# Kernel tuning notes

Hardware: AMD Instinct MI355X
Metric: run time of the kernel (lower is better)

## Reference

```python
import jax, jax.numpy as jnp
import numpy as np

DIM = 768
N_HEAD = 12
HEAD_DIM = 64
INNER = N_HEAD * HEAD_DIM
SCALE = HEAD_DIM ** -0.5


def setup_inputs() -> dict:
    key = jax.random.key(0)
    ks = jax.random.split(key, 12)
    B, Sf, St = 4, 2048, 2048
    from_tensor = jax.random.normal(ks[0], (B, Sf, DIM), dtype=jnp.float32)
    to_tensor = jax.random.normal(ks[1], (B, St, DIM), dtype=jnp.float32)
    attention_mask = jax.random.randint(ks[2], (B, Sf, St), 0, 2, dtype=jnp.int32)
    # Dense layers: kernel ~ RandomNormal (stddev 0.05, keras default), bias zeros
    def kern(k, fan_in, fan_out):
        return 0.05 * jax.random.normal(k, (fan_in, fan_out), dtype=jnp.float32)
    return {
        "from_tensor": from_tensor,
        "to_tensor": to_tensor,
        "attention_mask": attention_mask,
        "Wq": kern(ks[3], DIM, INNER), "bq": jnp.zeros((INNER,), jnp.float32),
        "Wk": kern(ks[4], DIM, INNER), "bk": jnp.zeros((INNER,), jnp.float32),
        "Wv": kern(ks[5], DIM, INNER), "bv": jnp.zeros((INNER,), jnp.float32),
        "Wo": kern(ks[6], INNER, DIM), "bo": jnp.zeros((DIM,), jnp.float32),
    }


def reference(from_tensor, to_tensor, attention_mask, Wq, bq, Wk, bk, Wv, bv, Wo, bo):
    B, Sf, _ = from_tensor.shape
    St = to_tensor.shape[1]
    # projections -> [B, S, n_head, head_dim] -> [B, n_head, S, head_dim]
    def split_heads(x, S):
        return x.reshape(B, S, N_HEAD, HEAD_DIM).transpose(0, 2, 1, 3)
    q = split_heads(from_tensor @ Wq + bq, Sf) * SCALE
    k = split_heads(to_tensor @ Wk + bk, St)
    v = split_heads(to_tensor @ Wv + bv, St)
    # scores [B, H, Sf, St]
    scores = jnp.einsum('bhik,bhjk->bhij', q, k)
    adder = (1.0 - attention_mask.astype(jnp.float32)) * -10000.0
    scores = scores + adder[:, None, :, :]
    probs = jax.nn.softmax(scores, axis=-1)
    out = jnp.einsum('bhij,bhjk->bhik', probs, v)  # [B, H, Sf, Dh]
    out = out.transpose(0, 2, 1, 3).reshape(B, Sf, INNER)
    return out @ Wo + bo
```

## Files before the change

kernel.cpp:

```cpp
#include <hip/hip_runtime.h>
#include <stdint.h>

#define DIM 768
#define NH 12
#define HD 64
#define BSZ 4
#define SEQ 2048
#define MROWS (BSZ*SEQ)

typedef __attribute__((ext_vector_type(8))) short v8s;
typedef __attribute__((ext_vector_type(4))) float v4f;
typedef __attribute__((ext_vector_type(8))) _Float16 v8h;
typedef __attribute__((ext_vector_type(2))) __fp16 v2fp;

__device__ __forceinline__ uint16_t f2bf(float x) {
  union { float f; uint32_t u; } v; v.f = x;
  uint32_t r = v.u + 0x7fffu + ((v.u >> 16) & 1u);
  return (uint16_t)(r >> 16);
}

#if __has_builtin(__builtin_amdgcn_cvt_pk_bf16_f32)
typedef __attribute__((ext_vector_type(2))) __bf16 v2bf;
__device__ __forceinline__ uint32_t pack_bf16(float a, float b) {
  union { v2bf v; uint32_t u; } c;
  c.v = __builtin_amdgcn_cvt_pk_bf16_f32(a, b);
  return c.u;
}
#else
__device__ __forceinline__ uint32_t pack_bf16(float a, float b) {
  return (uint32_t)f2bf(a) | ((uint32_t)f2bf(b) << 16);
}
#endif

__device__ __forceinline__ uint32_t pack_f16(float a, float b) {
#if __has_builtin(__builtin_amdgcn_cvt_pkrtz)
  union { v2fp h; uint32_t u; } c;
  c.h = __builtin_amdgcn_cvt_pkrtz(a, b);
  return c.u;
#else
  union { _Float16 h[2]; uint32_t u; } c;
  c.h[0] = (_Float16)a; c.h[1] = (_Float16)b; return c.u;
#endif
}

__device__ __forceinline__ float fexp2(float x) {
#if __has_builtin(__builtin_amdgcn_exp2f)
  return __builtin_amdgcn_exp2f(x);
#else
  return exp2f(x);
#endif
}

__device__ __forceinline__ void gl16(const void* g, void* l) {
  __builtin_amdgcn_global_load_lds(
      (const __attribute__((address_space(1))) unsigned int*)g,
      (__attribute__((address_space(3))) unsigned int*)l, 16, 0, 0);
}

__device__ __forceinline__ void pipe_sync() {
  asm volatile("s_waitcnt vmcnt(0)" ::: "memory");
  __builtin_amdgcn_s_barrier();
  __builtin_amdgcn_sched_barrier(0);
}

#define CVT_BLKS  12288
#define WT_BLKS   2304
__global__ __launch_bounds__(256) void prepass_kernel(
    const float* __restrict__ from_t, const float* __restrict__ to_t,
    uint16_t* __restrict__ Xf, uint16_t* __restrict__ Xt,
    const float* __restrict__ Wq, const float* __restrict__ Wk,
    const float* __restrict__ Wv, const float* __restrict__ Wo,
    uint16_t* __restrict__ WT)
{
  __shared__ float tile[32][33];
  int blk = blockIdx.x, tid = threadIdx.x;
  if (blk < CVT_BLKS) {
    int n4 = MROWS * DIM / 4;
    int i = blk * 256 + tid;
    const float* src = (i < n4) ? from_t : to_t;
    uint16_t* dst = (i < n4) ? Xf : Xt;
    int j = (i < n4) ? i : i - n4;
    float4 v = ((const float4*)src)[j];
    uint2 o;
    o.x = pack_bf16(v.x, v.y);
    o.y = pack_bf16(v.z, v.w);
    ((uint2*)dst)[j] = o;
  } else {
    int r = blk - CVT_BLKS;
    int z = r / 576, rem = r - z * 576;
    int by = rem / 24, bx = rem - by * 24;
    const float* src = (z==0) ? Wq : (z==1) ? Wk : (z==2) ? Wv : Wo;
    uint16_t* dst = WT + (size_t)z * DIM * DIM;
    int tx = tid & 31, ty = tid >> 5;
    int x  = bx * 32 + tx;
    int y0 = by * 32;
    for (int jj = ty; jj < 32; jj += 8)
      tile[jj][tx] = src[(size_t)(y0 + jj) * DIM + x];
    __syncthreads();
    int xo = y0 + tx;
    for (int jj = ty; jj < 32; jj += 8)
      dst[(size_t)(bx * 32 + jj) * DIM + xo] = f2bf(tile[tx][jj]);
  }
}

__global__ __launch_bounds__(256) void gemm_kernel(
    const uint16_t* __restrict__ Xf, const uint16_t* __restrict__ Xt,
    const uint16_t* __restrict__ WT, const uint16_t* __restrict__ AO,
    const float* __restrict__ bq, const float* __restrict__ bk,
    const float* __restrict__ bv, const float* __restrict__ bo,
    uint16_t* __restrict__ Qw, uint16_t* __restrict__ Kw, uint16_t* __restrict__ Vw,
    float* __restrict__ Out, const int* __restrict__ maski,
    unsigned long long* __restrict__ Mbits, int mode_base)
{
  __shared__ alignas(16) uint16_t As[2][128 * 32];
  __shared__ alignas(16) uint16_t Bs[2][128 * 32];
  int tid = threadIdx.x;

  if (mode_base == 0 && blockIdx.z == 3) {
    int wave = tid >> 6, lane = tid & 63;
    int wid = (blockIdx.y * 64 + blockIdx.x) * 4 + wave;
    const int NWAVES = 1536, NW = BSZ * 32 * SEQ;
    for (int w0 = wid; w0 < NW; w0 += 4 * NWAVES) {
      int m[4]; int wv[4];
      #pragma unroll
      for (int u = 0; u < 4; u++) {
        int w = w0 + u * NWAVES;
        wv[u] = w;
        m[u] = 0;
        if (w < NW) {
          int b  = w >> 16;
          int q  = (w >> 5) & 2047;
          int kt = w & 31;
          m[u] = maski[((size_t)b * SEQ + q) * SEQ + kt * 64 + lane];
        }
      }
      #pragma unroll
      for (int u = 0; u < 4; u++) {
        int w = wv[u];
        if (w < NW) {
          unsigned long long bits = __ballot(m[u] != 0);
          if (lane == 0) {
            int b  = w >> 16;
            int q  = (w >> 5) & 2047;
            int kt = w & 31;
            Mbits[((size_t)b * 32 + kt) * SEQ + q] = bits;
          }
        }
      }
    }
    return;
  }

  int mode = mode_base + blockIdx.z;
  const uint16_t* A = (mode == 0) ? Xf : (mode == 3 ? AO : Xt);
  const uint16_t* W = WT + (size_t)mode * DIM * DIM;
  const float* bias = (mode == 0) ? bq : (mode == 1) ? bk : (mode == 2) ? bv : bo;

  int m0 = blockIdx.x * 128, n0 = blockIdx.y * 128;
  int wave = tid >> 6, lane = tid & 63, lr = lane & 15, quad = lane >> 4;
  int wm = (wave >> 1) * 64, wn = (wave & 1) * 64;

  int seg = (lane & 3) ^ ((lane >> 3) & 3);
  const uint16_t* agl = A + (size_t)(m0 + wave * 32 + (lane >> 2)) * DIM + seg * 8;
  const uint16_t* bgl = W + (size_t)(n0 + wave * 32 + (lane >> 2)) * DIM + seg * 8;
  int lb = wave * 1024;
  int ck = (lr >> 1) & 3;

  v4f acc[4][4];
  v4f vz = {0.f, 0.f, 0.f, 0.f};
  #pragma unroll
  for (int i = 0; i < 4; i++)
    #pragma unroll
    for (int j = 0; j < 4; j++) acc[i][j] = vz;

  gl16(agl,            &As[0][lb]);
  gl16(agl + 16 * DIM, &As[0][lb + 512]);
  gl16(bgl,            &Bs[0][lb]);
  gl16(bgl + 16 * DIM, &Bs[0][lb + 512]);
  pipe_sync();

  int cur = 0;
  const int NT = DIM / 32;
  for (int t = 0; t < NT; ++t) {
    if (t + 1 < NT) {
      int kn = (t + 1) * 32;
      gl16(agl + kn,            &As[cur ^ 1][lb]);
      gl16(agl + kn + 16 * DIM, &As[cur ^ 1][lb + 512]);
      gl16(bgl + kn,            &Bs[cur ^ 1][lb]);
      gl16(bgl + kn + 16 * DIM, &Bs[cur ^ 1][lb + 512]);
    }
    v8s af[4], bfr[4];
    #pragma unroll
    for (int i = 0; i < 4; i++)
      af[i] = *(const v8s*)&As[cur][(wm + i * 16 + lr) * 32 + ((quad ^ ck) << 3)];
    #pragma unroll
    for (int j = 0; j < 4; j++)
      bfr[j] = *(const v8s*)&Bs[cur][(wn + j * 16 + lr) * 32 + ((quad ^ ck) << 3)];
    #pragma unroll
    for (int i = 0; i < 4; i++)
      #pragma unroll
      for (int j = 0; j < 4; j++)
        acc[i][j] = __builtin_amdgcn_mfma_f32_16x16x32_bf16(af[i], bfr[j], acc[i][j], 0, 0, 0);
    if (t + 1 < NT) pipe_sync();
    cur ^= 1;
  }

  float bj[4];
  #pragma unroll
  for (int j = 0; j < 4; j++) bj[j] = bias[n0 + wn + j * 16 + lr];

  if (mode == 3) {
    #pragma unroll
    for (int i = 0; i < 4; i++) {
      int m = m0 + wm + i * 16 + quad * 4;
      #pragma unroll
      for (int j = 0; j < 4; j++) {
        int n = n0 + wn + j * 16 + lr;
        #pragma unroll
        for (int r = 0; r < 4; r++)
          Out[(size_t)(m + r) * DIM + n] = acc[i][j][r] + bj[j];
      }
    }
  } else if (mode == 2) {
    #pragma unroll
    for (int i = 0; i < 4; i++) {
      int m = m0 + wm + i * 16 + quad * 4;
      int b = m >> 11, s0 = m & 2047;
      int kk0 = s0 & 63;
      int pos = (kk0 >> 5) * 32 + ((kk0 >> 2) & 3) * 8 + ((kk0 >> 4) & 1) * 4;
      int chunk = pos >> 3, off = pos & 7;
      #pragma unroll
      for (int j = 0; j < 4; j++) {
        int n = n0 + wn + j * 16 + lr;
        int h = n >> 6, d = n & 63;
        uint2 pk;
        pk.x = pack_f16(acc[i][j][0] + bj[j], acc[i][j][1] + bj[j]);
        pk.y = pack_f16(acc[i][j][2] + bj[j], acc[i][j][3] + bj[j]);
        int idx = (s0 & ~63) + ((chunk ^ (d & 7)) << 3) + off;
        *(uint2*)&Vw[((size_t)(b * NH + h) * HD + d) * SEQ + idx] = pk;
      }
    }
  } else {
    uint16_t* Dst = (mode == 0) ? Qw : Kw;
    float scale = (mode == 0) ? 0.18033688f : 1.0f;
    #pragma unroll
    for (int i = 0; i < 4; i++) {
      int m = m0 + wm + i * 16 + quad * 4;
      int b = m >> 11, s0 = m & 2047;
      #pragma unroll
      for (int j = 0; j < 4; j++) {
        int n = n0 + wn + j * 16 + lr;
        int h = n >> 6, d = n & 63;
        #pragma unroll
        for (int r = 0; r < 4; r++) {
          float v = (acc[i][j][r] + bj[j]) * scale;
          int s = s0 + r;
          int dd = (mode == 1) ? ((((d >> 3) ^ (s & 7)) << 3) + (d & 7)) : d;
          Dst[((size_t)(b * NH + h) * SEQ + s) * HD + dd] = f2bf(v);
        }
      }
    }
  }
}

__global__ __launch_bounds__(512, 6) void flash_kernel(
    const uint16_t* __restrict__ Qg, const uint16_t* __restrict__ Kg,
    const uint16_t* __restrict__ Vg, const unsigned long long* __restrict__ Mb,
    uint16_t* __restrict__ AO)
{
  __shared__ alignas(16) uint16_t Ks[2][64 * 64];
  __shared__ alignas(16) uint16_t Vs[2][64 * 64];

  int tid = threadIdx.x, wave = tid >> 6, lane = tid & 63, lr = lane & 15, quad = lane >> 4;

  int d = blockIdx.x + (blockIdx.y << 4);
  int nid = (d & 7) * 96 + (d >> 3);
  int bh = nid >> 4;
  int q0 = (nid & 15) * 128;
  int b = bh / NH, h = bh - b * NH;

  const uint16_t* Qp = Qg + (size_t)bh * SEQ * HD;
  const uint16_t* Kp = Kg + (size_t)bh * SEQ * HD;
  const uint16_t* Vp = Vg + (size_t)bh * HD * SEQ;
  int qg = q0 + wave * 16 + lr;
  const unsigned long long* Mp = Mb + (size_t)b * 32 * SEQ + qg;

  int swk = lr & 7, sh0 = quad * 4;

  v8s qfa = *(const v8s*)&Qp[(size_t)qg * HD + quad * 8];
  v8s qfb = *(const v8s*)&Qp[(size_t)qg * HD + 32 + quad * 8];

  const uint16_t* kgl = Kp + ((size_t)(wave * 8 + (lane >> 3)) * HD + (lane & 7) * 8);
  const uint16_t* vgl = Vp + ((size_t)(wave * 8 + (lane >> 3)) * SEQ + (lane & 7) * 8);
  int lb = wave * 512;

  v8h ones;
  #pragma unroll
  for (int i = 0; i < 8; i++) ones[i] = (_Float16)1.0f;

  v4f acc[4], lacc;
  v4f vz = {0.f, 0.f, 0.f, 0.f};
  v4f m8 = {-8.f, -8.f, -8.f, -8.f};
  #pragma unroll
  for (int dt = 0; dt < 4; dt++) acc[dt] = vz;
  lacc = vz;

  gl16(kgl, &Ks[0][lb]);
  gl16(vgl, &Vs[0][lb]);
  unsigned long long mw_cur = Mp[0];
  __syncthreads();

  int cur = 0;
  const int NT = SEQ / 64;
  for (int it = 0; it < NT; ++it) {
    unsigned long long mw_next = 0;
    if (it + 1 < NT) {
      int kn = (it + 1) * 64;
      gl16(kgl + (size_t)kn * HD, &Ks[cur ^ 1][lb]);
      gl16(vgl + kn,              &Vs[cur ^ 1][lb]);
      mw_next = Mp[(size_t)(it + 1) * SEQ];
    }

    uint32_t mlo = (uint32_t)mw_cur, mhi = (uint32_t)(mw_cur >> 32);
    v8h pf[2];
    #pragma unroll
    for (int p = 0; p < 2; p++) {
      v4f sA = m8, sB = m8;
      {
        int rowb = ((2 * p) * 16 + lr) << 6;
        v8s kf0 = *(const v8s*)&Ks[cur][rowb + ((quad ^ swk) << 3)];
        v8s kf1 = *(const v8s*)&Ks[cur][rowb + (((quad + 4) ^ swk) << 3)];
        sA = __builtin_amdgcn_mfma_f32_16x16x32_bf16(kf0, qfa, sA, 0, 0, 0);
        sA = __builtin_amdgcn_mfma_f32_16x16x32_bf16(kf1, qfb, sA, 0, 0, 0);
      }
      {
        int rowb = ((2 * p + 1) * 16 + lr) << 6;
        v8s kf0 = *(const v8s*)&Ks[cur][rowb + ((quad ^ swk) << 3)];
        v8s kf1 = *(const v8s*)&Ks[cur][rowb + (((quad + 4) ^ swk) << 3)];
        sB = __builtin_amdgcn_mfma_f32_16x16x32_bf16(kf0, qfa, sB, 0, 0, 0);
        sB = __builtin_amdgcn_mfma_f32_16x16x32_bf16(kf1, qfb, sB, 0, 0, 0);
      }
      uint32_t mword = p ? mhi : mlo;
      uint32_t b4a = (mword >> sh0) & 15u;
      uint32_t b4b = (mword >> (sh0 + 16)) & 15u;
      float ps[8];
      #pragma unroll
      for (int r = 0; r < 4; r++) {
        float ea = fexp2(sA[r]);
        float eb = fexp2(sB[r]);
        ps[r]     = (b4a & (1u << r)) ? ea : 0.0f;
        ps[4 + r] = (b4b & (1u << r)) ? eb : 0.0f;
      }
      union { uint4 u; v8h h; } cc;
      cc.u.x = pack_f16(ps[0], ps[1]);
      cc.u.y = pack_f16(ps[2], ps[3]);
      cc.u.z = pack_f16(ps[4], ps[5]);
      cc.u.w = pack_f16(ps[6], ps[7]);
      pf[p] = cc.h;
    }

    #pragma unroll
    for (int dt = 0; dt < 4; dt++) {
      int rowb = (dt * 16 + lr) << 6;
      #pragma unroll
      for (int p = 0; p < 2; p++) {
        v8h vv = *(const v8h*)&Vs[cur][rowb + (((p * 4 + quad) ^ swk) << 3)];
        acc[dt] = __builtin_amdgcn_mfma_f32_16x16x32_f16(vv, pf[p], acc[dt], 0, 0, 0);
      }
    }
    lacc = __builtin_amdgcn_mfma_f32_16x16x32_f16(ones, pf[0], lacc, 0, 0, 0);
    lacc = __builtin_amdgcn_mfma_f32_16x16x32_f16(ones, pf[1], lacc, 0, 0, 0);

    __syncthreads();
    mw_cur = mw_next;
    cur ^= 1;
  }

  float ri = 1.0f / lacc[0];

  #pragma unroll
  for (int dt = 0; dt < 4; dt++) {
    uint2 pk;
    pk.x = pack_bf16(acc[dt][0] * ri, acc[dt][1] * ri);
    pk.y = pack_bf16(acc[dt][2] * ri, acc[dt][3] * ri);
    *(uint2*)&AO[(size_t)(b * SEQ + qg) * DIM + h * HD + dt * 16 + sh0] = pk;
  }
}

extern "C" void kernel_launch(void* const* d_in, const int* in_sizes, int n_in,
                              void* d_out, int out_size, void* d_ws, size_t ws_size,
                              hipStream_t stream) {
  const float* from_t = (const float*)d_in[0];
  const float* to_t   = (const float*)d_in[1];
  const int*   maski  = (const int*)d_in[2];
  const float* Wq = (const float*)d_in[3];  const float* bq = (const float*)d_in[4];
  const float* Wk = (const float*)d_in[5];  const float* bk = (const float*)d_in[6];
  const float* Wv = (const float*)d_in[7];  const float* bv = (const float*)d_in[8];
  const float* Wo = (const float*)d_in[9];  const float* bo = (const float*)d_in[10];

  char* ws = (char*)d_ws;
  size_t off = 0;
  uint16_t* Xf = (uint16_t*)(ws + off); off += (size_t)MROWS * DIM * 2;
  uint16_t* Xt = (uint16_t*)(ws + off); off += (size_t)MROWS * DIM * 2;
  uint16_t* WT = (uint16_t*)(ws + off); off += (size_t)4 * DIM * DIM * 2;
  unsigned long long* Mbits = (unsigned long long*)(ws + off);
  off += (size_t)BSZ * 32 * SEQ * 8;
  uint16_t* Qw = (uint16_t*)(ws + off); off += (size_t)MROWS * DIM * 2;
  uint16_t* Kw = (uint16_t*)(ws + off); off += (size_t)MROWS * DIM * 2;
  uint16_t* Vw = (uint16_t*)(ws + off); off += (size_t)MROWS * DIM * 2;
  uint16_t* AO = (uint16_t*)(ws + off); off += (size_t)MROWS * DIM * 2;
  float* Out = (float*)d_out;

  prepass_kernel<<<CVT_BLKS + WT_BLKS, 256, 0, stream>>>(
      from_t, to_t, Xf, Xt, Wq, Wk, Wv, Wo, WT);

  gemm_kernel<<<dim3(64, 6, 4), 256, 0, stream>>>(Xf, Xt, WT, AO, bq, bk, bv, bo,
                                                  Qw, Kw, Vw, Out, maski, Mbits, 0);
  flash_kernel<<<dim3(SEQ / 128, BSZ * NH), 512, 0, stream>>>(Qw, Kw, Vw, Mbits, AO);
  gemm_kernel<<<dim3(64, 6, 1), 256, 0, stream>>>(Xf, Xt, WT, AO, bq, bk, bv, bo,
                                                  Qw, Kw, Vw, Out, maski, Mbits, 3);
}
```

Measured before the change: 364.8 us.

## Process two query row tiles per wave in flash kernel; split mask packing

The flash kernel now runs 4 waves of 256 threads per block, and each wave handles 32 query rows as two 16-row tiles. Each K and V fragment read from LDS is reused for both tiles, halving LDS reads per MFMA. Mask bit packing moves out of the fused QKV gemm launch into its own kernel, which removes the z==3 branch from the gemm. The trade-offs are higher register pressure per wave (launch bounds now 256,5), fewer waves per block to hide latency, and one extra kernel launch.

```diff
diff --git a/kernel.cpp b/kernel.cpp
--- a/kernel.cpp
+++ b/kernel.cpp
@@ -103,60 +103,37 @@
   }
 }
 
+__global__ void mask_bits_kernel(const int* __restrict__ src,
+                                 unsigned long long* __restrict__ dst, int nwords) {
+  int gtid = blockIdx.x * blockDim.x + threadIdx.x;
+  int w = gtid >> 6;
+  int lane = threadIdx.x & 63;
+  if (w >= nwords) return;
+  int b  = w >> 16;
+  int q  = (w >> 5) & 2047;
+  int kt = w & 31;
+  int m = src[((size_t)b * SEQ + q) * SEQ + kt * 64 + lane];
+  unsigned long long bits = __ballot(m != 0);
+  if (lane == 0) dst[((size_t)b * 32 + kt) * SEQ + q] = bits;
+}
+
 __global__ __launch_bounds__(256) void gemm_kernel(
     const uint16_t* __restrict__ Xf, const uint16_t* __restrict__ Xt,
     const uint16_t* __restrict__ WT, const uint16_t* __restrict__ AO,
     const float* __restrict__ bq, const float* __restrict__ bk,
     const float* __restrict__ bv, const float* __restrict__ bo,
     uint16_t* __restrict__ Qw, uint16_t* __restrict__ Kw, uint16_t* __restrict__ Vw,
-    float* __restrict__ Out, const int* __restrict__ maski,
-    unsigned long long* __restrict__ Mbits, int mode_base)
+    float* __restrict__ Out, int mode_base)
 {
   __shared__ alignas(16) uint16_t As[2][128 * 32];
   __shared__ alignas(16) uint16_t Bs[2][128 * 32];
-  int tid = threadIdx.x;
-
-  if (mode_base == 0 && blockIdx.z == 3) {
-    int wave = tid >> 6, lane = tid & 63;
-    int wid = (blockIdx.y * 64 + blockIdx.x) * 4 + wave;
-    const int NWAVES = 1536, NW = BSZ * 32 * SEQ;
-    for (int w0 = wid; w0 < NW; w0 += 4 * NWAVES) {
-      int m[4]; int wv[4];
-      #pragma unroll
-      for (int u = 0; u < 4; u++) {
-        int w = w0 + u * NWAVES;
-        wv[u] = w;
-        m[u] = 0;
-        if (w < NW) {
-          int b  = w >> 16;
-          int q  = (w >> 5) & 2047;
-          int kt = w & 31;
-          m[u] = maski[((size_t)b * SEQ + q) * SEQ + kt * 64 + lane];
-        }
-      }
-      #pragma unroll
-      for (int u = 0; u < 4; u++) {
-        int w = wv[u];
-        if (w < NW) {
-          unsigned long long bits = __ballot(m[u] != 0);
-          if (lane == 0) {
-            int b  = w >> 16;
-            int q  = (w >> 5) & 2047;
-            int kt = w & 31;
-            Mbits[((size_t)b * 32 + kt) * SEQ + q] = bits;
-          }
-        }
-      }
-    }
-    return;
-  }
-
   int mode = mode_base + blockIdx.z;
   const uint16_t* A = (mode == 0) ? Xf : (mode == 3 ? AO : Xt);
   const uint16_t* W = WT + (size_t)mode * DIM * DIM;
   const float* bias = (mode == 0) ? bq : (mode == 1) ? bk : (mode == 2) ? bv : bo;
 
   int m0 = blockIdx.x * 128, n0 = blockIdx.y * 128;
+  int tid = threadIdx.x;
   int wave = tid >> 6, lane = tid & 63, lr = lane & 15, quad = lane >> 4;
   int wm = (wave >> 1) * 64, wn = (wave & 1) * 64;
 
@@ -263,7 +240,7 @@
   }
 }
 
-__global__ __launch_bounds__(512, 6) void flash_kernel(
+__global__ __launch_bounds__(256, 5) void flash_kernel(
     const uint16_t* __restrict__ Qg, const uint16_t* __restrict__ Kg,
     const uint16_t* __restrict__ Vg, const unsigned long long* __restrict__ Mb,
     uint16_t* __restrict__ AO)
@@ -282,81 +259,99 @@
   const uint16_t* Qp = Qg + (size_t)bh * SEQ * HD;
   const uint16_t* Kp = Kg + (size_t)bh * SEQ * HD;
   const uint16_t* Vp = Vg + (size_t)bh * HD * SEQ;
-  int qg = q0 + wave * 16 + lr;
-  const unsigned long long* Mp = Mb + (size_t)b * 32 * SEQ + qg;
+  int qg0 = q0 + wave * 32 + lr;
+  int qg1 = qg0 + 16;
+  const unsigned long long* Mp0 = Mb + (size_t)b * 32 * SEQ + qg0;
+  const unsigned long long* Mp1 = Mp0 + 16;
 
   int swk = lr & 7, sh0 = quad * 4;
 
-  v8s qfa = *(const v8s*)&Qp[(size_t)qg * HD + quad * 8];
-  v8s qfb = *(const v8s*)&Qp[(size_t)qg * HD + 32 + quad * 8];
-
-  const uint16_t* kgl = Kp + ((size_t)(wave * 8 + (lane >> 3)) * HD + (lane & 7) * 8);
-  const uint16_t* vgl = Vp + ((size_t)(wave * 8 + (lane >> 3)) * SEQ + (lane & 7) * 8);
-  int lb = wave * 512;
+  v8s qf0a = *(const v8s*)&Qp[(size_t)qg0 * HD + quad * 8];
+  v8s qf0b = *(const v8s*)&Qp[(size_t)qg0 * HD + 32 + quad * 8];
+  v8s qf1a = *(const v8s*)&Qp[(size_t)qg1 * HD + quad * 8];
+  v8s qf1b = *(const v8s*)&Qp[(size_t)qg1 * HD + 32 + quad * 8];
+
+  const uint16_t* kgl = Kp + ((size_t)(wave * 16 + (lane >> 3)) * HD + (lane & 7) * 8);
+  const uint16_t* vgl = Vp + ((size_t)(wave * 16 + (lane >> 3)) * SEQ + (lane & 7) * 8);
+  int lb = wave * 1024;
 
   v8h ones;
   #pragma unroll
   for (int i = 0; i < 8; i++) ones[i] = (_Float16)1.0f;
 
-  v4f acc[4], lacc;
+  v4f acc0[4], acc1[4], lacc0, lacc1;
   v4f vz = {0.f, 0.f, 0.f, 0.f};
   v4f m8 = {-8.f, -8.f, -8.f, -8.f};
   #pragma unroll
-  for (int dt = 0; dt < 4; dt++) acc[dt] = vz;
-  lacc = vz;
-
-  gl16(kgl, &Ks[0][lb]);
-  gl16(vgl, &Vs[0][lb]);
-  unsigned long long mw_cur = Mp[0];
+  for (int dt = 0; dt < 4; dt++) { acc0[dt] = vz; acc1[dt] = vz; }
+  lacc0 = vz; lacc1 = vz;
+
+  gl16(kgl,                   &Ks[0][lb]);
+  gl16(kgl + (size_t)8 * HD,  &Ks[0][lb + 512]);
+  gl16(vgl,                   &Vs[0][lb]);
+  gl16(vgl + (size_t)8 * SEQ, &Vs[0][lb + 512]);
+  unsigned long long mw0_cur = Mp0[0];
+  unsigned long long mw1_cur = Mp1[0];
   __syncthreads();
 
   int cur = 0;
   const int NT = SEQ / 64;
   for (int it = 0; it < NT; ++it) {
-    unsigned long long mw_next = 0;
+    unsigned long long mw0_next = 0, mw1_next = 0;
     if (it + 1 < NT) {
       int kn = (it + 1) * 64;
-      gl16(kgl + (size_t)kn * HD, &Ks[cur ^ 1][lb]);
-      gl16(vgl + kn,              &Vs[cur ^ 1][lb]);
-      mw_next = Mp[(size_t)(it + 1) * SEQ];
-    }
-
-    uint32_t mlo = (uint32_t)mw_cur, mhi = (uint32_t)(mw_cur >> 32);
-    v8h pf[2];
+      gl16(kgl + (size_t)kn * HD,       &Ks[cur ^ 1][lb]);
+      gl16(kgl + (size_t)(kn + 8) * HD, &Ks[cur ^ 1][lb + 512]);
+      gl16(vgl + kn,                    &Vs[cur ^ 1][lb]);
+      gl16(vgl + kn + (size_t)8 * SEQ,  &Vs[cur ^ 1][lb + 512]);
+      mw0_next = Mp0[(size_t)(it + 1) * SEQ];
+      mw1_next = Mp1[(size_t)(it + 1) * SEQ];
+    }
+
+    uint32_t m0lo = (uint32_t)mw0_cur, m0hi = (uint32_t)(mw0_cur >> 32);
+    uint32_t m1lo = (uint32_t)mw1_cur, m1hi = (uint32_t)(mw1_cur >> 32);
+    v8h pf0[2], pf1[2];
     #pragma unroll
     for (int p = 0; p < 2; p++) {
-      v4f sA = m8, sB = m8;
+      v4f sA0 = m8, sB0 = m8, sA1 = m8, sB1 = m8;
       {
         int rowb = ((2 * p) * 16 + lr) << 6;
         v8s kf0 = *(const v8s*)&Ks[cur][rowb + ((quad ^ swk) << 3)];
         v8s kf1 = *(const v8s*)&Ks[cur][rowb + (((quad + 4) ^ swk) << 3)];
-        sA = __builtin_amdgcn_mfma_f32_16x16x32_bf16(kf0, qfa, sA, 0, 0, 0);
-        sA = __builtin_amdgcn_mfma_f32_16x16x32_bf16(kf1, qfb, sA, 0, 0, 0);
+        sA0 = __builtin_amdgcn_mfma_f32_16x16x32_bf16(kf0, qf0a, sA0, 0, 0, 0);
+        sA0 = __builtin_amdgcn_mfma_f32_16x16x32_bf16(kf1, qf0b, sA0, 0, 0, 0);
+        sA1 = __builtin_amdgcn_mfma_f32_16x16x32_bf16(kf0, qf1a, sA1, 0, 0, 0);
+        sA1 = __builtin_amdgcn_mfma_f32_16x16x32_bf16(kf1, qf1b, sA1, 0, 0, 0);
       }
       {
         int rowb = ((2 * p + 1) * 16 + lr) << 6;
         v8s kf0 = *(const v8s*)&Ks[cur][rowb + ((quad ^ swk) << 3)];
         v8s kf1 = *(const v8s*)&Ks[cur][rowb + (((quad + 4) ^ swk) << 3)];
-        sB = __builtin_amdgcn_mfma_f32_16x16x32_bf16(kf0, qfa, sB, 0, 0, 0);
-        sB = __builtin_amdgcn_mfma_f32_16x16x32_bf16(kf1, qfb, sB, 0, 0, 0);
-      }
-      uint32_t mword = p ? mhi : mlo;
-      uint32_t b4a = (mword >> sh0) & 15u;
-      uint32_t b4b = (mword >> (sh0 + 16)) & 15u;
-      float ps[8];
+        sB0 = __builtin_amdgcn_mfma_f32_16x16x32_bf16(kf0, qf0a, sB0, 0, 0, 0);
+        sB0 = __builtin_amdgcn_mfma_f32_16x16x32_bf16(kf1, qf0b, sB0, 0, 0, 0);
+        sB1 = __builtin_amdgcn_mfma_f32_16x16x32_bf16(kf0, qf1a, sB1, 0, 0, 0);
+        sB1 = __builtin_amdgcn_mfma_f32_16x16x32_bf16(kf1, qf1b, sB1, 0, 0, 0);
+      }
+      uint32_t w0 = p ? m0hi : m0lo, w1 = p ? m1hi : m1lo;
+      uint32_t a0 = (w0 >> sh0) & 15u, b0 = (w0 >> (sh0 + 16)) & 15u;
+      uint32_t a1 = (w1 >> sh0) & 15u, b1 = (w1 >> (sh0 + 16)) & 15u;
+      float p0[8], p1[8];
       #pragma unroll
       for (int r = 0; r < 4; r++) {
-        float ea = fexp2(sA[r]);
-        float eb = fexp2(sB[r]);
-        ps[r]     = (b4a & (1u << r)) ? ea : 0.0f;
-        ps[4 + r] = (b4b & (1u << r)) ? eb : 0.0f;
-      }
-      union { uint4 u; v8h h; } cc;
-      cc.u.x = pack_f16(ps[0], ps[1]);
-      cc.u.y = pack_f16(ps[2], ps[3]);
-      cc.u.z = pack_f16(ps[4], ps[5]);
-      cc.u.w = pack_f16(ps[6], ps[7]);
-      pf[p] = cc.h;
+        float e0a = fexp2(sA0[r]), e0b = fexp2(sB0[r]);
+        float e1a = fexp2(sA1[r]), e1b = fexp2(sB1[r]);
+        p0[r]     = (a0 & (1u << r)) ? e0a : 0.0f;
+        p0[4 + r] = (b0 & (1u << r)) ? e0b : 0.0f;
+        p1[r]     = (a1 & (1u << r)) ? e1a : 0.0f;
+        p1[4 + r] = (b1 & (1u << r)) ? e1b : 0.0f;
+      }
+      union { uint4 u; v8h h; } c0, c1;
+      c0.u.x = pack_f16(p0[0], p0[1]); c0.u.y = pack_f16(p0[2], p0[3]);
+      c0.u.z = pack_f16(p0[4], p0[5]); c0.u.w = pack_f16(p0[6], p0[7]);
+      c1.u.x = pack_f16(p1[0], p1[1]); c1.u.y = pack_f16(p1[2], p1[3]);
+      c1.u.z = pack_f16(p1[4], p1[5]); c1.u.w = pack_f16(p1[6], p1[7]);
+      pf0[p] = c0.h;
+      pf1[p] = c1.h;
     }
 
     #pragma unroll
@@ -365,25 +360,33 @@
       #pragma unroll
       for (int p = 0; p < 2; p++) {
         v8h vv = *(const v8h*)&Vs[cur][rowb + (((p * 4 + quad) ^ swk) << 3)];
-        acc[dt] = __builtin_amdgcn_mfma_f32_16x16x32_f16(vv, pf[p], acc[dt], 0, 0, 0);
-      }
-    }
-    lacc = __builtin_amdgcn_mfma_f32_16x16x32_f16(ones, pf[0], lacc, 0, 0, 0);
-    lacc = __builtin_amdgcn_mfma_f32_16x16x32_f16(ones, pf[1], lacc, 0, 0, 0);
+        acc0[dt] = __builtin_amdgcn_mfma_f32_16x16x32_f16(vv, pf0[p], acc0[dt], 0, 0, 0);
+        acc1[dt] = __builtin_amdgcn_mfma_f32_16x16x32_f16(vv, pf1[p], acc1[dt], 0, 0, 0);
+      }
+    }
+    lacc0 = __builtin_amdgcn_mfma_f32_16x16x32_f16(ones, pf0[0], lacc0, 0, 0, 0);
+    lacc0 = __builtin_amdgcn_mfma_f32_16x16x32_f16(ones, pf0[1], lacc0, 0, 0, 0);
+    lacc1 = __builtin_amdgcn_mfma_f32_16x16x32_f16(ones, pf1[0], lacc1, 0, 0, 0);
+    lacc1 = __builtin_amdgcn_mfma_f32_16x16x32_f16(ones, pf1[1], lacc1, 0, 0, 0);
 
     __syncthreads();
-    mw_cur = mw_next;
+    mw0_cur = mw0_next;
+    mw1_cur = mw1_next;
     cur ^= 1;
   }
 
-  float ri = 1.0f / lacc[0];
+  float ri0 = 1.0f / lacc0[0];
+  float ri1 = 1.0f / lacc1[0];
 
   #pragma unroll
   for (int dt = 0; dt < 4; dt++) {
     uint2 pk;
-    pk.x = pack_bf16(acc[dt][0] * ri, acc[dt][1] * ri);
-    pk.y = pack_bf16(acc[dt][2] * ri, acc[dt][3] * ri);
-    *(uint2*)&AO[(size_t)(b * SEQ + qg) * DIM + h * HD + dt * 16 + sh0] = pk;
+    pk.x = pack_bf16(acc0[dt][0] * ri0, acc0[dt][1] * ri0);
+    pk.y = pack_bf16(acc0[dt][2] * ri0, acc0[dt][3] * ri0);
+    *(uint2*)&AO[(size_t)(b * SEQ + qg0) * DIM + h * HD + dt * 16 + sh0] = pk;
+    pk.x = pack_bf16(acc1[dt][0] * ri1, acc1[dt][1] * ri1);
+    pk.y = pack_bf16(acc1[dt][2] * ri1, acc1[dt][3] * ri1);
+    *(uint2*)&AO[(size_t)(b * SEQ + qg1) * DIM + h * HD + dt * 16 + sh0] = pk;
   }
 }
 
@@ -413,10 +416,12 @@
 
   prepass_kernel<<<CVT_BLKS + WT_BLKS, 256, 0, stream>>>(
       from_t, to_t, Xf, Xt, Wq, Wk, Wv, Wo, WT);
-
-  gemm_kernel<<<dim3(64, 6, 4), 256, 0, stream>>>(Xf, Xt, WT, AO, bq, bk, bv, bo,
-                                                  Qw, Kw, Vw, Out, maski, Mbits, 0);
-  flash_kernel<<<dim3(SEQ / 128, BSZ * NH), 512, 0, stream>>>(Qw, Kw, Vw, Mbits, AO);
+  int nwords = BSZ * 32 * SEQ;
+  mask_bits_kernel<<<nwords * 64 / 256, 256, 0, stream>>>(maski, Mbits, nwords);
+
+  gemm_kernel<<<dim3(64, 6, 3), 256, 0, stream>>>(Xf, Xt, WT, AO, bq, bk, bv, bo,
+                                                  Qw, Kw, Vw, Out, 0);
+  flash_kernel<<<dim3(SEQ / 128, BSZ * NH), 256, 0, stream>>>(Qw, Kw, Vw, Mbits, AO);
   gemm_kernel<<<dim3(64, 6, 1), 256, 0, stream>>>(Xf, Xt, WT, AO, bq, bk, bv, bo,
-                                                  Qw, Kw, Vw, Out, maski, Mbits, 3);
-}
+                                                  Qw, Kw, Vw, Out, 3);
+}
```

Result: slower. 377.8 us (+3.6%).
